# Performance work log

Measured on AMD Instinct MI355X. Metric: run time of the kernel, lower is better.

The kernel has to match this reference:

```python
import jax, jax.numpy as jnp
import numpy as np

_MIN_BLOCK_KV = 32

def setup_inputs() -> dict:
    key = jax.random.key(0)
    k1, k2, k3, k4, k5, k6 = jax.random.split(key, 6)
    B, H, S, D = 256, 32, 16, 128  # batch, heads, max_kv_splits, head_dim
    att_out = jax.random.normal(k1, (B, H, S, D), dtype=jnp.float32)
    att_lse = jax.random.normal(k2, (B, H, S), dtype=jnp.float32)
    q = jax.random.normal(k3, (B, H, D), dtype=jnp.float32)
    v_buffer = jax.random.normal(k4, (1024, D), dtype=jnp.float32)  # only last dim (Lv) is used
    # Ragged per-batch KV lengths in [32, 8192]; strictly positive so every batch has >=1 valid split.
    kv_lens = jax.random.randint(k5, (B,), 32, 8193, dtype=jnp.int32)
    kv_indptr = jnp.concatenate([jnp.zeros((1,), jnp.int32), jnp.cumsum(kv_lens).astype(jnp.int32)])
    num_kv_splits = jax.random.randint(k6, (B,), 1, S + 1, dtype=jnp.int32)
    return {"att_out": att_out, "att_lse": att_lse, "q": q, "v_buffer": v_buffer,
            "kv_indptr": kv_indptr, "num_kv_splits": num_kv_splits}

def reference(att_out, att_lse, q, v_buffer, kv_indptr, num_kv_splits):
    # Split-KV (flash-decoding) stage-2 merge: combine per-split partial
    # attention outputs using their partial logsumexp stats.
    B, H, S, D = att_out.shape
    seq_len = kv_indptr[1:] - kv_indptr[:-1]                      # [B]
    splits = num_kv_splits                                        # [B]
    per_split = -(-(-(-seq_len // splits)) // _MIN_BLOCK_KV) * _MIN_BLOCK_KV  # cdiv(cdiv(len,splits),32)*32
    split_start = per_split[:, None] * jnp.arange(S, dtype=seq_len.dtype)[None, :]  # [B,S]
    valid = split_start < seq_len[:, None]                        # [B,S] split contributes iff start < seq_len
    lse = jnp.where(valid[:, None, :], att_lse, -jnp.inf)         # [B,H,S]
    m = jnp.max(lse, axis=-1, keepdims=True)                      # [B,H,1]
    w = jnp.exp(lse - m)                                          # invalid splits -> 0
    e_sum = jnp.sum(w, axis=-1)                                   # [B,H]
    o = jnp.einsum('bhs,bhsd->bhd', w, att_out) / e_sum[..., None]
    return o.astype(att_out.dtype)
```

## Files before the change

kernel.cpp:

```cpp
#include <hip/hip_runtime.h>
#include <hip/hip_bf16.h>
#include <math.h>

#define NB 256
#define NH 32
#define NS 16
#define ND 128

__global__ __launch_bounds__(256) void merge_splits_kernel(
    const float* __restrict__ att_out,
    const float* __restrict__ att_lse,
    const int*   __restrict__ kv_indptr,
    const int*   __restrict__ num_splits,
    float*       __restrict__ out)
{
    const int wid  = threadIdx.x >> 6;
    const int lane = threadIdx.x & 63;
    const int half = lane >> 5;
    const int l    = lane & 31;
    const int row  = blockIdx.x * 8 + wid * 2 + half;
    const int b    = row >> 5;

    const int seq_len = kv_indptr[b + 1] - kv_indptr[b];
    const int splits  = num_splits[b];
    int ps = (seq_len + splits - 1) / splits;
    ps = ((ps + 31) >> 5) << 5;
    const int nvalid = (seq_len + ps - 1) / ps;

    const float4* lse4 = (const float4*)(att_lse + (size_t)row * NS);
    const float4 L0 = lse4[0], L1 = lse4[1], L2 = lse4[2], L3 = lse4[3];
    float w[NS] = {L0.x, L0.y, L0.z, L0.w, L1.x, L1.y, L1.z, L1.w,
                   L2.x, L2.y, L2.z, L2.w, L3.x, L3.y, L3.z, L3.w};

    float m = -INFINITY;
#pragma unroll
    for (int s = 0; s < NS; ++s) {
        const float li = (s < nvalid) ? w[s] : -INFINITY;
        w[s] = li;
        m = fmaxf(m, li);
    }
    float esum = 0.f;
#pragma unroll
    for (int s = 0; s < NS; ++s) {
        w[s] = __expf(w[s] - m);
        esum += w[s];
    }

    const float4* __restrict__ src =
        (const float4*)(att_out + (size_t)row * NS * ND);
    float4 v[NS];
#pragma unroll
    for (int s = 0; s < NS; ++s) v[s] = make_float4(0.f, 0.f, 0.f, 0.f);
#pragma unroll
    for (int s = 0; s < NS; ++s) {
        if (s < nvalid) v[s] = src[s * (ND / 4) + l];
    }

    float4 acc = make_float4(0.f, 0.f, 0.f, 0.f);
#pragma unroll
    for (int s = 0; s < NS; ++s) {
        acc.x = fmaf(w[s], v[s].x, acc.x);
        acc.y = fmaf(w[s], v[s].y, acc.y);
        acc.z = fmaf(w[s], v[s].z, acc.z);
        acc.w = fmaf(w[s], v[s].w, acc.w);
    }

    const float inv = 1.f / esum;
    float4* dst = (float4*)(out + (size_t)row * ND);
    dst[l] = make_float4(acc.x * inv, acc.y * inv, acc.z * inv, acc.w * inv);
}

extern "C" void kernel_launch(void* const* d_in, const int* in_sizes, int n_in,
                              void* d_out, int out_size, void* d_ws, size_t ws_size,
                              hipStream_t stream) {
    const float* att_out    = (const float*)d_in[0];
    const float* att_lse    = (const float*)d_in[1];
    const int*   kv_indptr  = (const int*)d_in[4];
    const int*   num_splits = (const int*)d_in[5];
    float* out = (float*)d_out;

    const int rows = NB * NH;
    const int blocks = rows / 8;
    merge_splits_kernel<<<blocks, 256, 0, stream>>>(
        att_out, att_lse, kv_indptr, num_splits, out);
}
```

Before: 11.51 us.

## Split each row's splits across wave halves and combine with cross-lane shuffles

Each 64-lane wave now handles one output row instead of two. The two 32-lane halves take the even and odd splits, and partial max, sum and accumulators are merged with __shfl_xor. This halves the per-thread load count and register footprint (8 float4 instead of 16), which should raise memory-level parallelism and occupancy. Launch bounds are tightened to request more resident blocks. The cost is twice as many blocks, extra shuffles, and half the lanes going idle at the store.

```diff
diff --git a/kernel.cpp b/kernel.cpp
--- a/kernel.cpp
+++ b/kernel.cpp
@@ -7,18 +7,19 @@
 #define NS 16
 #define ND 128
 
-__global__ __launch_bounds__(256) void merge_splits_kernel(
+__global__ __launch_bounds__(256, 8) void merge_splits_kernel(
     const float* __restrict__ att_out,
     const float* __restrict__ att_lse,
     const int*   __restrict__ kv_indptr,
     const int*   __restrict__ num_splits,
     float*       __restrict__ out)
 {
-    const int wid  = threadIdx.x >> 6;
-    const int lane = threadIdx.x & 63;
+    const int tid  = threadIdx.x;
+    const int wid  = tid >> 6;
+    const int lane = tid & 63;
     const int half = lane >> 5;
     const int l    = lane & 31;
-    const int row  = blockIdx.x * 8 + wid * 2 + half;
+    const int row  = blockIdx.x * 4 + wid;
     const int b    = row >> 5;
 
     const int seq_len = kv_indptr[b + 1] - kv_indptr[b];
@@ -26,48 +27,67 @@
     int ps = (seq_len + splits - 1) / splits;
     ps = ((ps + 31) >> 5) << 5;
     const int nvalid = (seq_len + ps - 1) / ps;
+    const int nvm1   = nvalid - 1;
 
     const float4* lse4 = (const float4*)(att_lse + (size_t)row * NS);
     const float4 L0 = lse4[0], L1 = lse4[1], L2 = lse4[2], L3 = lse4[3];
-    float w[NS] = {L0.x, L0.y, L0.z, L0.w, L1.x, L1.y, L1.z, L1.w,
-                   L2.x, L2.y, L2.z, L2.w, L3.x, L3.y, L3.z, L3.w};
+
+    const float4* __restrict__ src =
+        (const float4*)(att_out + (size_t)row * NS * ND);
+    float4 v[8];
+#pragma unroll
+    for (int p = 0; p < 8; ++p) {
+        if (2 * p < nvalid) {
+            const int sp = 2 * p + half;
+            const int sc = (sp <= nvm1) ? sp : nvm1;
+            v[p] = src[sc * (ND / 4) + l];
+        }
+    }
+
+    float w[8];
+    w[0] = half ? L0.y : L0.x;  w[1] = half ? L0.w : L0.z;
+    w[2] = half ? L1.y : L1.x;  w[3] = half ? L1.w : L1.z;
+    w[4] = half ? L2.y : L2.x;  w[5] = half ? L2.w : L2.z;
+    w[6] = half ? L3.y : L3.x;  w[7] = half ? L3.w : L3.z;
 
     float m = -INFINITY;
 #pragma unroll
-    for (int s = 0; s < NS; ++s) {
-        const float li = (s < nvalid) ? w[s] : -INFINITY;
-        w[s] = li;
+    for (int p = 0; p < 8; ++p) {
+        const float li = (2 * p + half < nvalid) ? w[p] : -INFINITY;
+        w[p] = li;
         m = fmaxf(m, li);
     }
+    m = fmaxf(m, __shfl_xor(m, 32));
+
     float esum = 0.f;
 #pragma unroll
-    for (int s = 0; s < NS; ++s) {
-        w[s] = __expf(w[s] - m);
-        esum += w[s];
-    }
-
-    const float4* __restrict__ src =
-        (const float4*)(att_out + (size_t)row * NS * ND);
-    float4 v[NS];
-#pragma unroll
-    for (int s = 0; s < NS; ++s) v[s] = make_float4(0.f, 0.f, 0.f, 0.f);
-#pragma unroll
-    for (int s = 0; s < NS; ++s) {
-        if (s < nvalid) v[s] = src[s * (ND / 4) + l];
+    for (int p = 0; p < 8; ++p) {
+        w[p] = __expf(w[p] - m);
+        esum += w[p];
     }
 
     float4 acc = make_float4(0.f, 0.f, 0.f, 0.f);
 #pragma unroll
-    for (int s = 0; s < NS; ++s) {
-        acc.x = fmaf(w[s], v[s].x, acc.x);
-        acc.y = fmaf(w[s], v[s].y, acc.y);
-        acc.z = fmaf(w[s], v[s].z, acc.z);
-        acc.w = fmaf(w[s], v[s].w, acc.w);
+    for (int p = 0; p < 8; ++p) {
+        if (2 * p < nvalid) {
+            acc.x = fmaf(w[p], v[p].x, acc.x);
+            acc.y = fmaf(w[p], v[p].y, acc.y);
+            acc.z = fmaf(w[p], v[p].z, acc.z);
+            acc.w = fmaf(w[p], v[p].w, acc.w);
+        }
     }
 
-    const float inv = 1.f / esum;
-    float4* dst = (float4*)(out + (size_t)row * ND);
-    dst[l] = make_float4(acc.x * inv, acc.y * inv, acc.z * inv, acc.w * inv);
+    esum  += __shfl_xor(esum, 32);
+    acc.x += __shfl_xor(acc.x, 32);
+    acc.y += __shfl_xor(acc.y, 32);
+    acc.z += __shfl_xor(acc.z, 32);
+    acc.w += __shfl_xor(acc.w, 32);
+
+    if (half == 0) {
+        const float inv = 1.f / esum;
+        float4* dst = (float4*)(out + (size_t)row * ND);
+        dst[l] = make_float4(acc.x * inv, acc.y * inv, acc.z * inv, acc.w * inv);
+    }
 }
 
 extern "C" void kernel_launch(void* const* d_in, const int* in_sizes, int n_in,
@@ -80,7 +100,7 @@
     float* out = (float*)d_out;
 
     const int rows = NB * NH;
-    const int blocks = rows / 8;
+    const int blocks = rows / 4;
     merge_splits_kernel<<<blocks, 256, 0, stream>>>(
         att_out, att_lse, kv_indptr, num_splits, out);
 }
```

Result: faster. 10.92 us (-5.2%).
